# Performance work log

Measured on AMD Instinct MI355X. Metric: run time of the kernel, lower is better.

The kernel has to match this reference:

```python
import jax, jax.numpy as jnp
import numpy as np

E = 16           # num_experts
D = 4096         # hidden_size
F = 688          # per-expert SwiGLU intermediate size
N = 8192         # total tokens (bsz*seq_len)
CAP_FACTOR = 1.25


def setup_inputs() -> dict:
    key = jax.random.key(0)
    k1, k2, k3, k4, k5, k6 = jax.random.split(key, 6)
    return {
        "x": jax.random.normal(k1, (N, D), dtype=jnp.float32),
        "topk_idx": jax.random.randint(k2, (N,), 0, E, dtype=jnp.int32),
        "topk_scores": jax.random.uniform(k3, (N,), dtype=jnp.float32),
        "Wg": jax.random.normal(k4, (E, D, F), dtype=jnp.float32) * 0.02,
        "Wu": jax.random.normal(k5, (E, D, F), dtype=jnp.float32) * 0.02,
        "Wd": jax.random.normal(k6, (E, F, D), dtype=jnp.float32) * 0.02,
    }


def reference(x, topk_idx, topk_scores, Wg, Wu, Wd):
    # Switch-style top-1 MoE with capacity-based token dropping.
    # Deterministic variant: tokens beyond capacity are dropped in token order
    # (original uses randperm; the math pattern is identical).
    n, d = x.shape
    e = Wg.shape[0]
    cap = int(CAP_FACTOR * n / e)  # static under jit

    # position of each token within its assigned expert (0-based)
    oh = jax.nn.one_hot(topk_idx, e, dtype=jnp.int32)            # [N, E]
    pos = jnp.take_along_axis(jnp.cumsum(oh, axis=0) - 1,
                              topk_idx[:, None].astype(jnp.int32), axis=1)[:, 0]
    keep = pos < cap                                             # [N] bool

    # dispatch: scatter kept tokens into [E, cap, D]; dropped go to dummy row E
    e_safe = jnp.where(keep, topk_idx, e)
    p_safe = jnp.minimum(pos, cap - 1)
    buf = jnp.zeros((e + 1, cap, d), x.dtype).at[e_safe, p_safe].set(x)[:e]

    # per-expert SwiGLU FFN: down(silu(gate(x)) * up(x))
    h = jax.nn.silu(jnp.einsum('ecd,edf->ecf', buf, Wg)) \
        * jnp.einsum('ecd,edf->ecf', buf, Wu)                    # [E, cap, F]
    out = jnp.einsum('ecf,efd->ecd', h, Wd)                      # [E, cap, D]

    # combine: gather back, zero-pad dropped tokens, scale by gate scores
    y = out[topk_idx, p_safe] * keep[:, None].astype(x.dtype)
    y = y * topk_scores[:, None]
    return y
```

## Files before the change

### kernel.cpp

```cpp
#include <hip/hip_runtime.h>
#include <hip/hip_bf16.h>

#define E_ 16
#define D_ 4096
#define F_ 688
#define N_ 8192
#define CAP_ 640
#define NKT_ 64
#define NFT_ 11

typedef __attribute__((ext_vector_type(8))) short bf16x8;
typedef __attribute__((ext_vector_type(4))) float f32x4;
typedef __attribute__((ext_vector_type(4))) float fvec4;
typedef __attribute__((ext_vector_type(8))) unsigned short usvec8;

__device__ __forceinline__ unsigned short f2bf(float f) {
    __hip_bfloat16 h = __float2bfloat16(f);
    return __builtin_bit_cast(unsigned short, h);
}
__device__ __forceinline__ int lidx(int row, int k) {
    return row * 64 + (((k >> 3) ^ (row & 7)) << 3) + (k & 7);
}
__device__ __forceinline__ int bidx(int row, int k) {
    return row * 64 + (((k >> 3) ^ ((row >> 1) & 7)) << 3) + (k & 7);
}
__device__ __forceinline__ void gload16(const unsigned short* g, unsigned short* l) {
    __builtin_amdgcn_global_load_lds(
        (const __attribute__((address_space(1))) unsigned int*)g,
        (__attribute__((address_space(3))) unsigned int*)l, 16, 0, 0);
}

__global__ void k_dispatch(const int* __restrict__ idx,
                           int* __restrict__ slot_token,
                           int* __restrict__ row_of,
                           int* __restrict__ cnt) {
    __shared__ int hist[256][E_];
    const int t = threadIdx.x;
#pragma unroll
    for (int e = 0; e < E_; e++) hist[t][e] = 0;
    __syncthreads();
    const int base = t * (N_ / 256);
    for (int j = 0; j < N_ / 256; j++) {
        int e = idx[base + j];
        hist[t][e]++;
    }
    __syncthreads();
    if (t < E_) {
        int run = 0;
        for (int i = 0; i < 256; i++) { int v = hist[i][t]; hist[i][t] = run; run += v; }
        cnt[t] = run < CAP_ ? run : CAP_;
    }
    for (int s = t; s < E_ * CAP_; s += 256) slot_token[s] = -1;
    __syncthreads();
    for (int j = 0; j < N_ / 256; j++) {
        int i = base + j;
        int e = idx[i];
        int p = hist[t][e]++;
        if (p < CAP_) { slot_token[e * CAP_ + p] = i; row_of[i] = e * CAP_ + p; }
        else          { row_of[i] = -1; }
    }
}

__global__ void k_zero_dropped(const int* __restrict__ row_of, float* __restrict__ y) {
    const int i = blockIdx.x;
    if (row_of[i] >= 0) return;
    fvec4* yp = (fvec4*)(y + (size_t)i * D_);
    fvec4 z = {0.f, 0.f, 0.f, 0.f};
    for (int c = threadIdx.x; c < D_ / 4; c += 256) yp[c] = z;
}

__global__ void k_gather(const float* __restrict__ x, const int* __restrict__ slot_token,
                         unsigned short* __restrict__ Aimg) {
    const int strip = blockIdx.y;
    const int kg = blockIdx.x;
    const int t = threadIdx.x;
    const int r = t >> 1, h = t & 1;
    const int tok = slot_token[strip * 128 + r];
#pragma unroll
    for (int kl4 = 0; kl4 < 4; kl4++) {
        const int kt = kg * 4 + kl4;
        const int k0 = kt * 64 + h * 32;
        unsigned short* dst = Aimg + ((size_t)strip * NKT_ + kt) * 8192;
        usvec8 p[4];
        if (tok < 0) {
            usvec8 z = {0, 0, 0, 0, 0, 0, 0, 0};
            p[0] = z; p[1] = z; p[2] = z; p[3] = z;
        } else {
            const float* src = x + (size_t)tok * D_ + k0;
#pragma unroll
            for (int uu = 0; uu < 4; uu++) {
                fvec4 a = *(const fvec4*)(src + uu * 8);
                fvec4 b = *(const fvec4*)(src + uu * 8 + 4);
                usvec8 q = {f2bf(a[0]), f2bf(a[1]), f2bf(a[2]), f2bf(a[3]),
                            f2bf(b[0]), f2bf(b[1]), f2bf(b[2]), f2bf(b[3])};
                p[uu] = q;
            }
        }
#pragma unroll
        for (int uu = 0; uu < 4; uu++)
            *(usvec8*)&dst[lidx(r, h * 32 + uu * 8)] = p[uu];
    }
}

#define WAITV(N) asm volatile("s_waitcnt vmcnt(" #N ")" ::: "memory")
#define WAITL    asm volatile("s_waitcnt lgkmcnt(0)" ::: "memory")
#define SBAR     __builtin_amdgcn_s_barrier()
#define SCHED0   __builtin_amdgcn_sched_barrier(0)

__global__ __launch_bounds__(256, 2) void k_gemm1(
    const unsigned short* __restrict__ Aimg,
    const float* __restrict__ Wg, const float* __restrict__ Wu,
    const int* __restrict__ cnt, unsigned short* __restrict__ Himg) {
    const int bid = blockIdx.x;
    const int xcd = bid & 7;
    const int j = bid >> 3;
    const int mb = j % 5;
    const int gl = j / 5;
    const int group = xcd * 22 + gl;
    const int e = group / NFT_, fidx = group % NFT_;
    const int m0 = mb * 128, f0 = fidx * 64;
    if (m0 >= cnt[e]) return;
    const int strip = e * 5 + mb;

    __shared__ __align__(16) unsigned short As[3][128 * 64];
    __shared__ __align__(16) unsigned short Bgs[2][64 * 64];
    __shared__ __align__(16) unsigned short Bus[2][64 * 64];

    const int tid = threadIdx.x;
    const int lane = tid & 63, wave = tid >> 6;
    const int wm = wave >> 1, wn = wave & 1;

    f32x4 accG[4][2], accU[4][2];
#pragma unroll
    for (int a = 0; a < 4; a++)
#pragma unroll
        for (int b = 0; b < 2; b++) {
            f32x4 z = {0.f, 0.f, 0.f, 0.f};
            accG[a][b] = z; accU[a][b] = z;
        }

    const int fpos = (tid & 31) * 2, kq8 = (tid >> 5) * 8;
    const int gf = f0 + fpos;
    const bool bvalid = gf < F_;
    const float2 fz2 = {0.f, 0.f};
    const float* WgE = Wg + (size_t)e * D_ * F_;
    const float* WuE = Wu + (size_t)e * D_ * F_;
    const unsigned short* Astrip = Aimg + (size_t)strip * NKT_ * 8192;
    const int aoff0 = wave * 4 * 512;

    {
        float2 g[8], u[8];
#pragma unroll
        for (int r = 0; r < 8; r++) {
            size_t off = (size_t)(kq8 + r) * F_ + gf;
            g[r] = bvalid ? *(const float2*)(WgE + off) : fz2;
            u[r] = bvalid ? *(const float2*)(WuE + off) : fz2;
        }
#pragma unroll
        for (int i = 0; i < 4; i++)
            gload16(Astrip + aoff0 + i * 512 + lane * 8, &As[0][aoff0 + i * 512]);
#pragma unroll
        for (int i = 0; i < 4; i++)
            gload16(Astrip + 8192 + aoff0 + i * 512 + lane * 8, &As[1][aoff0 + i * 512]);
        usvec8 pg0, pg1, pu0, pu1;
#pragma unroll
        for (int r = 0; r < 8; r++) {
            pg0[r] = (short)f2bf(g[r].x); pg1[r] = (short)f2bf(g[r].y);
            pu0[r] = (short)f2bf(u[r].x); pu1[r] = (short)f2bf(u[r].y);
        }
        *(usvec8*)&Bgs[0][bidx(fpos, kq8)]     = pg0;
        *(usvec8*)&Bgs[0][bidx(fpos + 1, kq8)] = pg1;
        *(usvec8*)&Bus[0][bidx(fpos, kq8)]     = pu0;
        *(usvec8*)&Bus[0][bidx(fpos + 1, kq8)] = pu1;
    }
    WAITV(4);
    WAITL;
    SBAR;
    SCHED0;

    for (int kt = 0; kt < NKT_; ++kt) {
        const int cur3 = kt % 3, curb = kt & 1;
        const bool hb = (kt + 1 < NKT_), ha = (kt + 2 < NKT_);
        float2 g[8], u[8];
        if (hb) {
#pragma unroll
            for (int r = 0; r < 8; r++) {
                size_t off = ((size_t)(kt + 1) * 64 + kq8 + r) * F_ + gf;
                g[r] = bvalid ? *(const float2*)(WgE + off) : fz2;
                u[r] = bvalid ? *(const float2*)(WuE + off) : fz2;
            }
        }
        if (ha) {
            const unsigned short* asrc = Astrip + (size_t)(kt + 2) * 8192 + aoff0;
            unsigned short* adst = &As[(kt + 2) % 3][aoff0];
#pragma unroll
            for (int i = 0; i < 4; i++)
                gload16(asrc + i * 512 + lane * 8, adst + i * 512);
        }
        SCHED0;
        __builtin_amdgcn_s_setprio(1);
#pragma unroll
        for (int kk = 0; kk < 64; kk += 32) {
            const int ko = kk + ((lane >> 4) << 3);
            bf16x8 av[4], bgv[2], buv[2];
#pragma unroll
            for (int mi = 0; mi < 4; mi++)
                av[mi] = *(const bf16x8*)&As[cur3][lidx(wm * 64 + mi * 16 + (lane & 15), ko)];
#pragma unroll
            for (int ni = 0; ni < 2; ni++) {
                int rr = wn * 32 + ni * 16 + (lane & 15);
                bgv[ni] = *(const bf16x8*)&Bgs[curb][bidx(rr, ko)];
                buv[ni] = *(const bf16x8*)&Bus[curb][bidx(rr, ko)];
            }
#pragma unroll
            for (int mi = 0; mi < 4; mi++)
#pragma unroll
                for (int ni = 0; ni < 2; ni++) {
                    accG[mi][ni] = __builtin_amdgcn_mfma_f32_16x16x32_bf16(av[mi], bgv[ni], accG[mi][ni], 0, 0, 0);
                    accU[mi][ni] = __builtin_amdgcn_mfma_f32_16x16x32_bf16(av[mi], buv[ni], accU[mi][ni], 0, 0, 0);
                }
        }
        __builtin_amdgcn_s_setprio(0);
        SCHED0;
        if (hb) {
            usvec8 pg0, pg1, pu0, pu1;
#pragma unroll
            for (int r = 0; r < 8; r++) {
                pg0[r] = (short)f2bf(g[r].x); pg1[r] = (short)f2bf(g[r].y);
                pu0[r] = (short)f2bf(u[r].x); pu1[r] = (short)f2bf(u[r].y);
            }
            const int nb = curb ^ 1;
            *(usvec8*)&Bgs[nb][bidx(fpos, kq8)]     = pg0;
            *(usvec8*)&Bgs[nb][bidx(fpos + 1, kq8)] = pg1;
            *(usvec8*)&Bus[nb][bidx(fpos, kq8)]     = pu0;
            *(usvec8*)&Bus[nb][bidx(fpos + 1, kq8)] = pu1;
        }
        if (ha) WAITV(4); else WAITV(0);
        WAITL;
        SBAR;
        SCHED0;
    }

    unsigned short* Ht = Himg + ((size_t)strip * NFT_ + fidx) * 8192;
#pragma unroll
    for (int mi = 0; mi < 4; mi++)
#pragma unroll
        for (int ni = 0; ni < 2; ni++) {
            int fl = wn * 32 + ni * 16 + (lane & 15);
            int rl = wm * 64 + mi * 16 + ((lane >> 4) << 2);
#pragma unroll
            for (int q = 0; q < 4; q++) {
                float g = accG[mi][ni][q], u = accU[mi][ni][q];
                float h = g * u / (1.f + __expf(-g));
                Ht[lidx(rl + q, fl)] = f2bf(h);
            }
        }
}

__global__ __launch_bounds__(256, 2) void k_gemm2(
    const unsigned short* __restrict__ Himg, const float* __restrict__ Wd,
    const int* __restrict__ slot_token, const int* __restrict__ cnt,
    const float* __restrict__ scores, float* __restrict__ y) {
    const int bid = blockIdx.x;
    const int xcd = bid & 7;
    const int j = bid >> 3;
    const int mb = j % 5;
    const int gl = j / 5;
    const int group = xcd * 128 + gl;
    const int e = group >> 6, didx = group & 63;
    const int m0 = mb * 128, d0 = didx * 64;
    if (m0 >= cnt[e]) return;
    const int strip = e * 5 + mb;

    __shared__ __align__(16) unsigned short As[3][128 * 64];
    __shared__ __align__(16) unsigned short Bts[2][64 * 64];
    __shared__ int tokS[128];
    __shared__ float scS[128];

    const int tid = threadIdx.x;
    const int lane = tid & 63, wave = tid >> 6;
    const int wm = wave >> 1, wn = wave & 1;

    if (tid < 128) {
        int t = slot_token[e * CAP_ + m0 + tid];
        tokS[tid] = t;
        scS[tid] = (t >= 0) ? scores[t] : 0.f;
    }

    f32x4 acc[4][2];
#pragma unroll
    for (int a = 0; a < 4; a++)
#pragma unroll
        for (int b = 0; b < 2; b++) {
            f32x4 z = {0.f, 0.f, 0.f, 0.f};
            acc[a][b] = z;
        }

    const int dpos = (tid & 31) * 2, kq8 = (tid >> 5) * 8;
    const int gd = d0 + dpos;
    const float2 fz2 = {0.f, 0.f};
    const float* WdE = Wd + (size_t)e * F_ * D_;
    const unsigned short* Hstrip = Himg + (size_t)strip * NFT_ * 8192;
    const int aoff0 = wave * 4 * 512;

    {
        float2 b[8];
#pragma unroll
        for (int r = 0; r < 8; r++) {
            int kr = kq8 + r;
            b[r] = (kr < F_) ? *(const float2*)(WdE + (size_t)kr * D_ + gd) : fz2;
        }
#pragma unroll
        for (int i = 0; i < 4; i++)
            gload16(Hstrip + aoff0 + i * 512 + lane * 8, &As[0][aoff0 + i * 512]);
#pragma unroll
        for (int i = 0; i < 4; i++)
            gload16(Hstrip + 8192 + aoff0 + i * 512 + lane * 8, &As[1][aoff0 + i * 512]);
        usvec8 p0, p1;
#pragma unroll
        for (int r = 0; r < 8; r++) { p0[r] = (short)f2bf(b[r].x); p1[r] = (short)f2bf(b[r].y); }
        *(usvec8*)&Bts[0][bidx(dpos, kq8)]     = p0;
        *(usvec8*)&Bts[0][bidx(dpos + 1, kq8)] = p1;
    }
    WAITV(4);
    WAITL;
    SBAR;
    SCHED0;

    for (int fc = 0; fc < NFT_; ++fc) {
        const int cur3 = fc % 3, curb = fc & 1;
        const bool hb = (fc + 1 < NFT_), ha = (fc + 2 < NFT_);
        float2 b[8];
        if (hb) {
#pragma unroll
            for (int r = 0; r < 8; r++) {
                int kr = (fc + 1) * 64 + kq8 + r;
                b[r] = (kr < F_) ? *(const float2*)(WdE + (size_t)kr * D_ + gd) : fz2;
            }
        }
        if (ha) {
            const unsigned short* asrc = Hstrip + (size_t)(fc + 2) * 8192 + aoff0;
            unsigned short* adst = &As[(fc + 2) % 3][aoff0];
#pragma unroll
            for (int i = 0; i < 4; i++)
                gload16(asrc + i * 512 + lane * 8, adst + i * 512);
        }
        SCHED0;
        __builtin_amdgcn_s_setprio(1);
#pragma unroll
        for (int kk = 0; kk < 64; kk += 32) {
            const int ko = kk + ((lane >> 4) << 3);
            bf16x8 av[4], bv[2];
#pragma unroll
            for (int mi = 0; mi < 4; mi++)
                av[mi] = *(const bf16x8*)&As[cur3][lidx(wm * 64 + mi * 16 + (lane & 15), ko)];
#pragma unroll
            for (int ni = 0; ni < 2; ni++)
                bv[ni] = *(const bf16x8*)&Bts[curb][bidx(wn * 32 + ni * 16 + (lane & 15), ko)];
#pragma unroll
            for (int mi = 0; mi < 4; mi++)
#pragma unroll
                for (int ni = 0; ni < 2; ni++)
                    acc[mi][ni] = __builtin_amdgcn_mfma_f32_16x16x32_bf16(av[mi], bv[ni], acc[mi][ni], 0, 0, 0);
        }
        __builtin_amdgcn_s_setprio(0);
        SCHED0;
        if (hb) {
            usvec8 p0, p1;
#pragma unroll
            for (int r = 0; r < 8; r++) { p0[r] = (short)f2bf(b[r].x); p1[r] = (short)f2bf(b[r].y); }
            const int nb = curb ^ 1;
            *(usvec8*)&Bts[nb][bidx(dpos, kq8)]     = p0;
            *(usvec8*)&Bts[nb][bidx(dpos + 1, kq8)] = p1;
        }
        if (ha) WAITV(4); else WAITV(0);
        WAITL;
        SBAR;
        SCHED0;
    }

#pragma unroll
    for (int mi = 0; mi < 4; mi++)
#pragma unroll
        for (int ni = 0; ni < 2; ni++) {
            int d = d0 + wn * 32 + ni * 16 + (lane & 15);
            int rowb = wm * 64 + mi * 16 + ((lane >> 4) << 2);
#pragma unroll
            for (int q = 0; q < 4; q++) {
                int row = rowb + q;
                int t = tokS[row];
                if (t >= 0) y[(size_t)t * D_ + d] = acc[mi][ni][q] * scS[row];
            }
        }
}

extern "C" void kernel_launch(void* const* d_in, const int* in_sizes, int n_in,
                              void* d_out, int out_size, void* d_ws, size_t ws_size,
                              hipStream_t stream) {
    const float* x   = (const float*)d_in[0];
    const int*   idx = (const int*)d_in[1];
    const float* sc  = (const float*)d_in[2];
    const float* Wg  = (const float*)d_in[3];
    const float* Wu  = (const float*)d_in[4];
    const float* Wd  = (const float*)d_in[5];
    float* y = (float*)d_out;

    char* ws = (char*)d_ws;
    int* slot_token = (int*)ws;
    int* row_of     = (int*)(ws + 40960);
    int* cnt        = (int*)(ws + 40960 + 32768);
    const size_t hoff = 131072;
    const size_t hbytes = (size_t)80 * NFT_ * 8192 * 2;
    unsigned short* Himg = (unsigned short*)(ws + hoff);
    const size_t aoff = hoff + hbytes;
    unsigned short* Aimg = (unsigned short*)(ws + aoff);

    k_dispatch<<<1, 256, 0, stream>>>(idx, slot_token, row_of, cnt);
    k_zero_dropped<<<N_, 256, 0, stream>>>(row_of, y);
    k_gather<<<dim3(16, 80), 256, 0, stream>>>(x, slot_token, Aimg);
    k_gemm1<<<880, 256, 0, stream>>>(Aimg, Wg, Wu, cnt, Himg);
    k_gemm2<<<5120, 256, 0, stream>>>(Himg, Wd, slot_token, cnt, sc, y);
}
```

Before: 520.9 us.

## Pre-convert weights to swizzled bf16 images and load GEMM tiles via LDS DMA

Adds per-call kernels that convert Wg/Wu/Wd from fp32 into swizzled bf16 tile images in workspace. New GEMM kernels then stream both operands with global_load_lds and a triple-buffered pipeline, instead of loading fp32 weights through registers and converting them. This removes the repeated fp32 conversion and register staging, at the cost of an extra full read and write pass over the weights. The new path only runs if the workspace is large enough; otherwise it falls back to the old kernels.

Result: slower. 730.9 us (+40.3%).

```diff
diff --git a/kernel.cpp b/kernel.cpp
--- a/kernel.cpp
+++ b/kernel.cpp
@@ -29,6 +29,11 @@
         (const __attribute__((address_space(1))) unsigned int*)g,
         (__attribute__((address_space(3))) unsigned int*)l, 16, 0, 0);
 }
+
+#define WAITV(N) asm volatile("s_waitcnt vmcnt(" #N ")" ::: "memory")
+#define WAITL    asm volatile("s_waitcnt lgkmcnt(0)" ::: "memory")
+#define SBAR     __builtin_amdgcn_s_barrier()
+#define SCHED0   __builtin_amdgcn_sched_barrier(0)
 
 __global__ void k_dispatch(const int* __restrict__ idx,
                            int* __restrict__ slot_token,
@@ -102,12 +107,258 @@
     }
 }
 
-#define WAITV(N) asm volatile("s_waitcnt vmcnt(" #N ")" ::: "memory")
-#define WAITL    asm volatile("s_waitcnt lgkmcnt(0)" ::: "memory")
-#define SBAR     __builtin_amdgcn_s_barrier()
-#define SCHED0   __builtin_amdgcn_sched_barrier(0)
-
-__global__ __launch_bounds__(256, 2) void k_gemm1(
+__global__ void k_wprep_gu(const float* __restrict__ Wg, const float* __restrict__ Wu,
+                           unsigned short* __restrict__ img) {
+    const int ft = blockIdx.x, kt = blockIdx.y, e = blockIdx.z;
+    const int tid = threadIdx.x;
+    const int fpos = (tid & 31) * 2, kq8 = (tid >> 5) * 8;
+    const int gf = ft * 64 + fpos;
+    const bool v = gf < F_;
+    const float2 fz2 = {0.f, 0.f};
+    float2 g[8], u[8];
+#pragma unroll
+    for (int r = 0; r < 8; r++) {
+        size_t off = (size_t)e * D_ * F_ + (size_t)(kt * 64 + kq8 + r) * F_ + gf;
+        g[r] = v ? *(const float2*)(Wg + off) : fz2;
+        u[r] = v ? *(const float2*)(Wu + off) : fz2;
+    }
+    usvec8 pg0, pg1, pu0, pu1;
+#pragma unroll
+    for (int r = 0; r < 8; r++) {
+        pg0[r] = (short)f2bf(g[r].x); pg1[r] = (short)f2bf(g[r].y);
+        pu0[r] = (short)f2bf(u[r].x); pu1[r] = (short)f2bf(u[r].y);
+    }
+    unsigned short* t = img + ((size_t)(e * NKT_ + kt) * NFT_ + ft) * 8192;
+    *(usvec8*)&t[bidx(fpos, kq8)]            = pg0;
+    *(usvec8*)&t[bidx(fpos + 1, kq8)]        = pg1;
+    *(usvec8*)&t[4096 + bidx(fpos, kq8)]     = pu0;
+    *(usvec8*)&t[4096 + bidx(fpos + 1, kq8)] = pu1;
+}
+
+__global__ void k_wprep_d(const float* __restrict__ Wd, unsigned short* __restrict__ img) {
+    const int dt = blockIdx.x, kt = blockIdx.y, e = blockIdx.z;
+    const int tid = threadIdx.x;
+    const int dpos = (tid & 31) * 2, kq8 = (tid >> 5) * 8;
+    const int gd = dt * 64 + dpos;
+    const float2 fz2 = {0.f, 0.f};
+    float2 b[8];
+#pragma unroll
+    for (int r = 0; r < 8; r++) {
+        int krow = kt * 64 + kq8 + r;
+        b[r] = (krow < F_) ? *(const float2*)(Wd + (size_t)e * F_ * D_ + (size_t)krow * D_ + gd) : fz2;
+    }
+    usvec8 p0, p1;
+#pragma unroll
+    for (int r = 0; r < 8; r++) { p0[r] = (short)f2bf(b[r].x); p1[r] = (short)f2bf(b[r].y); }
+    unsigned short* t = img + ((size_t)(e * NFT_ + kt) * 64 + dt) * 4096;
+    *(usvec8*)&t[bidx(dpos, kq8)]     = p0;
+    *(usvec8*)&t[bidx(dpos + 1, kq8)] = p1;
+}
+
+__global__ __launch_bounds__(256, 1) void k_gemm1_dma(
+    const unsigned short* __restrict__ Aimg, const unsigned short* __restrict__ Wgu,
+    const int* __restrict__ cnt, unsigned short* __restrict__ Himg) {
+    const int bid = blockIdx.x;
+    const int xcd = bid & 7;
+    const int j = bid >> 3;
+    const int mb = j % 5;
+    const int gl = j / 5;
+    const int group = xcd * 22 + gl;
+    const int e = group / NFT_, fidx = group % NFT_;
+    const int m0 = mb * 128, f0 = fidx * 64;
+    if (m0 >= cnt[e]) return;
+    const int strip = e * 5 + mb;
+
+    __shared__ __align__(16) unsigned short As[3][8192];
+    __shared__ __align__(16) unsigned short Bgs[3][4096];
+    __shared__ __align__(16) unsigned short Bus[3][4096];
+
+    const int tid = threadIdx.x;
+    const int lane = tid & 63, wave = tid >> 6;
+    const int wm = wave >> 1, wn = wave & 1;
+    const int aw4 = wave * 4, bw2 = wave * 2;
+
+    f32x4 accG[4][2], accU[4][2];
+#pragma unroll
+    for (int a = 0; a < 4; a++)
+#pragma unroll
+        for (int b = 0; b < 2; b++) {
+            f32x4 z = {0.f, 0.f, 0.f, 0.f};
+            accG[a][b] = z; accU[a][b] = z;
+        }
+
+    const unsigned short* Astrip = Aimg + (size_t)strip * NKT_ * 8192;
+    const unsigned short* WguE = Wgu + (size_t)e * NKT_ * NFT_ * 8192 + (size_t)fidx * 8192;
+
+#define G1STAGE(T, BUF)                                                        \
+    {                                                                          \
+        const unsigned short* asrc = Astrip + (size_t)(T) * 8192;              \
+        _Pragma("unroll") for (int i = 0; i < 4; i++)                          \
+            gload16(asrc + (aw4 + i) * 512 + lane * 8, &As[BUF][(aw4 + i) * 512]); \
+        const unsigned short* bsrc = WguE + (size_t)(T) * (NFT_ * 8192);       \
+        _Pragma("unroll") for (int i = 0; i < 2; i++)                          \
+            gload16(bsrc + (bw2 + i) * 512 + lane * 8, &Bgs[BUF][(bw2 + i) * 512]); \
+        _Pragma("unroll") for (int i = 0; i < 2; i++)                          \
+            gload16(bsrc + 4096 + (bw2 + i) * 512 + lane * 8, &Bus[BUF][(bw2 + i) * 512]); \
+    }
+
+    G1STAGE(0, 0)
+    G1STAGE(1, 1)
+    WAITV(8);
+    SBAR;
+
+    for (int kt = 0; kt < NKT_; ++kt) {
+        const int cur = kt % 3;
+        if (kt + 2 < NKT_) G1STAGE(kt + 2, (kt + 2) % 3)
+        SCHED0;
+        __builtin_amdgcn_s_setprio(1);
+#pragma unroll
+        for (int kk = 0; kk < 64; kk += 32) {
+            const int ko = kk + ((lane >> 4) << 3);
+            bf16x8 av[4], bgv[2], buv[2];
+#pragma unroll
+            for (int mi = 0; mi < 4; mi++)
+                av[mi] = *(const bf16x8*)&As[cur][lidx(wm * 64 + mi * 16 + (lane & 15), ko)];
+#pragma unroll
+            for (int ni = 0; ni < 2; ni++) {
+                int rr = wn * 32 + ni * 16 + (lane & 15);
+                bgv[ni] = *(const bf16x8*)&Bgs[cur][bidx(rr, ko)];
+                buv[ni] = *(const bf16x8*)&Bus[cur][bidx(rr, ko)];
+            }
+#pragma unroll
+            for (int mi = 0; mi < 4; mi++)
+#pragma unroll
+                for (int ni = 0; ni < 2; ni++) {
+                    accG[mi][ni] = __builtin_amdgcn_mfma_f32_16x16x32_bf16(av[mi], bgv[ni], accG[mi][ni], 0, 0, 0);
+                    accU[mi][ni] = __builtin_amdgcn_mfma_f32_16x16x32_bf16(av[mi], buv[ni], accU[mi][ni], 0, 0, 0);
+                }
+        }
+        __builtin_amdgcn_s_setprio(0);
+        SCHED0;
+        if (kt + 2 < NKT_) WAITV(8); else WAITV(0);
+        if (kt + 1 < NKT_) SBAR;
+    }
+#undef G1STAGE
+
+    unsigned short* Ht = Himg + ((size_t)strip * NFT_ + fidx) * 8192;
+#pragma unroll
+    for (int mi = 0; mi < 4; mi++)
+#pragma unroll
+        for (int ni = 0; ni < 2; ni++) {
+            int fl = wn * 32 + ni * 16 + (lane & 15);
+            int rl = wm * 64 + mi * 16 + ((lane >> 4) << 2);
+#pragma unroll
+            for (int q = 0; q < 4; q++) {
+                float g = accG[mi][ni][q], u = accU[mi][ni][q];
+                float h = g * u / (1.f + __expf(-g));
+                Ht[lidx(rl + q, fl)] = f2bf(h);
+            }
+        }
+}
+
+__global__ __launch_bounds__(256, 2) void k_gemm2_dma(
+    const unsigned short* __restrict__ Himg, const unsigned short* __restrict__ WdI,
+    const int* __restrict__ slot_token, const int* __restrict__ cnt,
+    const float* __restrict__ scores, float* __restrict__ y) {
+    const int bid = blockIdx.x;
+    const int xcd = bid & 7;
+    const int j = bid >> 3;
+    const int mb = j % 5;
+    const int gl = j / 5;
+    const int group = xcd * 128 + gl;
+    const int e = group >> 6, didx = group & 63;
+    const int m0 = mb * 128, d0 = didx * 64;
+    if (m0 >= cnt[e]) return;
+    const int strip = e * 5 + mb;
+
+    __shared__ __align__(16) unsigned short As[3][8192];
+    __shared__ __align__(16) unsigned short Bts[3][4096];
+    __shared__ int tokS[128];
+    __shared__ float scS[128];
+
+    const int tid = threadIdx.x;
+    const int lane = tid & 63, wave = tid >> 6;
+    const int wm = wave >> 1, wn = wave & 1;
+    const int aw4 = wave * 4, bw2 = wave * 2;
+
+    if (tid < 128) {
+        int t = slot_token[e * CAP_ + m0 + tid];
+        tokS[tid] = t;
+        scS[tid] = (t >= 0) ? scores[t] : 0.f;
+    }
+    __syncthreads();
+
+    f32x4 acc[4][2];
+#pragma unroll
+    for (int a = 0; a < 4; a++)
+#pragma unroll
+        for (int b = 0; b < 2; b++) {
+            f32x4 z = {0.f, 0.f, 0.f, 0.f};
+            acc[a][b] = z;
+        }
+
+    const unsigned short* Hstrip = Himg + (size_t)strip * NFT_ * 8192;
+    const unsigned short* WdE = WdI + (size_t)e * NFT_ * 64 * 4096 + (size_t)didx * 4096;
+
+#define G2STAGE(T, BUF)                                                        \
+    {                                                                          \
+        const unsigned short* asrc = Hstrip + (size_t)(T) * 8192;              \
+        _Pragma("unroll") for (int i = 0; i < 4; i++)                          \
+            gload16(asrc + (aw4 + i) * 512 + lane * 8, &As[BUF][(aw4 + i) * 512]); \
+        const unsigned short* bsrc = WdE + (size_t)(T) * (64 * 4096);          \
+        _Pragma("unroll") for (int i = 0; i < 2; i++)                          \
+            gload16(bsrc + (bw2 + i) * 512 + lane * 8, &Bts[BUF][(bw2 + i) * 512]); \
+    }
+
+    G2STAGE(0, 0)
+    G2STAGE(1, 1)
+    WAITV(6);
+    SBAR;
+
+    for (int fc = 0; fc < NFT_; ++fc) {
+        const int cur = fc % 3;
+        if (fc + 2 < NFT_) G2STAGE(fc + 2, (fc + 2) % 3)
+        SCHED0;
+        __builtin_amdgcn_s_setprio(1);
+#pragma unroll
+        for (int kk = 0; kk < 64; kk += 32) {
+            const int ko = kk + ((lane >> 4) << 3);
+            bf16x8 av[4], bv[2];
+#pragma unroll
+            for (int mi = 0; mi < 4; mi++)
+                av[mi] = *(const bf16x8*)&As[cur][lidx(wm * 64 + mi * 16 + (lane & 15), ko)];
+#pragma unroll
+            for (int ni = 0; ni < 2; ni++)
+                bv[ni] = *(const bf16x8*)&Bts[cur][bidx(wn * 32 + ni * 16 + (lane & 15), ko)];
+#pragma unroll
+            for (int mi = 0; mi < 4; mi++)
+#pragma unroll
+                for (int ni = 0; ni < 2; ni++)
+                    acc[mi][ni] = __builtin_amdgcn_mfma_f32_16x16x32_bf16(av[mi], bv[ni], acc[mi][ni], 0, 0, 0);
+        }
+        __builtin_amdgcn_s_setprio(0);
+        SCHED0;
+        if (fc + 2 < NFT_) WAITV(6); else WAITV(0);
+        if (fc + 1 < NFT_) SBAR;
+    }
+#undef G2STAGE
+
+#pragma unroll
+    for (int mi = 0; mi < 4; mi++)
+#pragma unroll
+        for (int ni = 0; ni < 2; ni++) {
+            int d = d0 + wn * 32 + ni * 16 + (lane & 15);
+            int rowb = wm * 64 + mi * 16 + ((lane >> 4) << 2);
+#pragma unroll
+            for (int q = 0; q < 4; q++) {
+                int row = rowb + q;
+                int t = tokS[row];
+                if (t >= 0) y[(size_t)t * D_ + d] = acc[mi][ni][q] * scS[row];
+            }
+        }
+}
+
+__global__ __launch_bounds__(256, 2) void k_gemm1_rs(
     const unsigned short* __restrict__ Aimg,
     const float* __restrict__ Wg, const float* __restrict__ Wu,
     const int* __restrict__ cnt, unsigned short* __restrict__ Himg) {
@@ -122,9 +373,9 @@
     if (m0 >= cnt[e]) return;
     const int strip = e * 5 + mb;
 
-    __shared__ __align__(16) unsigned short As[3][128 * 64];
-    __shared__ __align__(16) unsigned short Bgs[2][64 * 64];
-    __shared__ __align__(16) unsigned short Bus[2][64 * 64];
+    __shared__ __align__(16) unsigned short As[3][8192];
+    __shared__ __align__(16) unsigned short Bgs[2][4096];
+    __shared__ __align__(16) unsigned short Bus[2][4096];
 
     const int tid = threadIdx.x;
     const int lane = tid & 63, wave = tid >> 6;
@@ -257,7 +508,7 @@
         }
 }
 
-__global__ __launch_bounds__(256, 2) void k_gemm2(
+__global__ __launch_bounds__(256, 2) void k_gemm2_rs(
     const unsigned short* __restrict__ Himg, const float* __restrict__ Wd,
     const int* __restrict__ slot_token, const int* __restrict__ cnt,
     const float* __restrict__ scores, float* __restrict__ y) {
@@ -272,8 +523,8 @@
     if (m0 >= cnt[e]) return;
     const int strip = e * 5 + mb;
 
-    __shared__ __align__(16) unsigned short As[3][128 * 64];
-    __shared__ __align__(16) unsigned short Bts[2][64 * 64];
+    __shared__ __align__(16) unsigned short As[3][8192];
+    __shared__ __align__(16) unsigned short Bts[2][4096];
     __shared__ int tokS[128];
     __shared__ float scS[128];
 
@@ -409,15 +660,30 @@
     int* slot_token = (int*)ws;
     int* row_of     = (int*)(ws + 40960);
     int* cnt        = (int*)(ws + 40960 + 32768);
-    const size_t hoff = 131072;
-    const size_t hbytes = (size_t)80 * NFT_ * 8192 * 2;
+    const size_t hoff   = 131072;
+    const size_t hbytes = (size_t)80 * NFT_ * 16384;
     unsigned short* Himg = (unsigned short*)(ws + hoff);
-    const size_t aoff = hoff + hbytes;
+    const size_t aoff   = hoff + hbytes;
+    const size_t abytes = (size_t)80 * NKT_ * 16384;
     unsigned short* Aimg = (unsigned short*)(ws + aoff);
+    const size_t guoff   = aoff + abytes;
+    const size_t gubytes = (size_t)E_ * NKT_ * NFT_ * 16384;
+    unsigned short* WguI = (unsigned short*)(ws + guoff);
+    const size_t wdoff   = guoff + gubytes;
+    const size_t wdbytes = (size_t)E_ * NFT_ * 64 * 8192;
+    unsigned short* WdI  = (unsigned short*)(ws + wdoff);
+    const bool full = ws_size >= wdoff + wdbytes;
 
     k_dispatch<<<1, 256, 0, stream>>>(idx, slot_token, row_of, cnt);
     k_zero_dropped<<<N_, 256, 0, stream>>>(row_of, y);
     k_gather<<<dim3(16, 80), 256, 0, stream>>>(x, slot_token, Aimg);
-    k_gemm1<<<880, 256, 0, stream>>>(Aimg, Wg, Wu, cnt, Himg);
-    k_gemm2<<<5120, 256, 0, stream>>>(Himg, Wd, slot_token, cnt, sc, y);
-}
+    if (full) {
+        k_wprep_gu<<<dim3(NFT_, NKT_, E_), 256, 0, stream>>>(Wg, Wu, WguI);
+        k_wprep_d<<<dim3(64, NFT_, E_), 256, 0, stream>>>(Wd, WdI);
+        k_gemm1_dma<<<880, 256, 0, stream>>>(Aimg, WguI, cnt, Himg);
+        k_gemm2_dma<<<5120, 256, 0, stream>>>(Himg, WdI, slot_token, cnt, sc, y);
+    } else {
+        k_gemm1_rs<<<880, 256, 0, stream>>>(Aimg, Wg, Wu, cnt, Himg);
+        k_gemm2_rs<<<5120, 256, 0, stream>>>(Himg, Wd, slot_token, cnt, sc, y);
+    }
+}
```
